# Kernel tuning notes

Hardware: AMD Instinct MI355X
Metric: run time of the kernel (lower is better)

The kernel has to match this reference:

```python
import jax, jax.numpy as jnp
import numpy as np

N = 100000   # nodes
E = 1000000  # edges
DIN = 128    # atom_in_features
DE = 16      # edge_attr_dim
H = 128      # hidden width (preprocess/cheb/postprocess)
K = 3        # Chebyshev order
EPS = 1e-5


def setup_inputs() -> dict:
    key = jax.random.key(0)
    ks = jax.random.split(key, 16)
    s = 0.02
    return {
        "x": jax.random.normal(ks[0], (N, DIN), jnp.float32),
        "edge_index": jax.random.randint(ks[1], (2, E), 0, N),
        "edge_attr": jax.random.normal(ks[2], (E, DE), jnp.float32),
        # AtomEdgeInteraction linear: (DIN+DE) -> H
        "w_int": jax.random.normal(ks[3], (DIN + DE, H), jnp.float32) * s,
        "b_int": jnp.zeros((H,), jnp.float32),
        # preprocess layer 1: Linear + BatchNorm + ReLU
        "w_pre": jax.random.normal(ks[4], (H, H), jnp.float32) * s,
        "b_pre": jnp.zeros((H,), jnp.float32),
        "g_pre": jnp.ones((H,), jnp.float32),
        "be_pre": jnp.zeros((H,), jnp.float32),
        # ChebConv layers: weight [K, in, out] + bias
        "cheb1_w": jax.random.normal(ks[5], (K, H, H), jnp.float32) * s,
        "cheb1_b": jnp.zeros((H,), jnp.float32),
        "cheb2_w": jax.random.normal(ks[6], (K, H, H), jnp.float32) * s,
        "cheb2_b": jnp.zeros((H,), jnp.float32),
        # postprocess: Linear + BatchNorm + ReLU
        "w_post": jax.random.normal(ks[7], (H, H), jnp.float32) * s,
        "b_post": jnp.zeros((H,), jnp.float32),
        "g_post": jnp.ones((H,), jnp.float32),
        "be_post": jnp.zeros((H,), jnp.float32),
        # output layer H -> 1
        "w_out": jax.random.normal(ks[8], (H, 1), jnp.float32) * s,
        "b_out": jnp.zeros((1,), jnp.float32),
    }


def _bn(z, g, b):
    # BatchNorm1d, training-mode batch statistics (biased variance, like torch)
    m = z.mean(0)
    v = ((z - m) ** 2).mean(0)
    return g * (z - m) * jax.lax.rsqrt(v + EPS) + b


def _cheb(h, W, b, row, col, norm):
    # ChebConv with sym normalization, lambda_max=2 => L_hat = -D^{-1/2} A D^{-1/2}
    def lhat(z):
        return jax.ops.segment_sum(norm[:, None] * z[row], col, num_segments=N)

    Tx0 = h
    out = Tx0 @ W[0]
    Tx1 = lhat(Tx0)
    out = out + Tx1 @ W[1]
    for k in range(2, W.shape[0]):
        Tx2 = 2.0 * lhat(Tx1) - Tx0
        out = out + Tx2 @ W[k]
        Tx0, Tx1 = Tx1, Tx2
    return out + b


def reference(x, edge_index, edge_attr,
              w_int, b_int,
              w_pre, b_pre, g_pre, be_pre,
              cheb1_w, cheb1_b, cheb2_w, cheb2_b,
              w_post, b_post, g_post, be_post,
              w_out, b_out):
    row, col = edge_index[0], edge_index[1]
    ones_e = jnp.ones((E,), x.dtype)

    # AtomEdgeInteraction: gather -> concat -> linear -> scatter_mean over col
    comb = jnp.concatenate([x[row], edge_attr], axis=-1)  # [E, DIN+DE]
    upd = comb @ w_int + b_int                             # [E, H]
    cnt = jax.ops.segment_sum(ones_e, col, num_segments=N)
    h = jax.ops.segment_sum(upd, col, num_segments=N) / jnp.clip(cnt, 1.0)[:, None]

    # preprocess layer 1 (Linear + BN + ReLU; dropout rate 0)
    h = jax.nn.relu(_bn(h @ w_pre + b_pre, g_pre, be_pre))

    # sym-normalized edge coefficients for scaled Laplacian
    deg = jax.ops.segment_sum(ones_e, row, num_segments=N)
    dis = jnp.where(deg > 0, jax.lax.rsqrt(jnp.maximum(deg, 1.0)), 0.0)
    norm = -dis[row] * dis[col]  # [E]

    h = jax.nn.relu(_cheb(h, cheb1_w, cheb1_b, row, col, norm))
    h = jax.nn.relu(_cheb(h, cheb2_w, cheb2_b, row, col, norm))

    # postprocess (Linear + BN + ReLU)
    h = jax.nn.relu(_bn(h @ w_post + b_post, g_post, be_post))

    # output layer, squeeze(-1) -> [N]
    return (h @ w_out + b_out).squeeze(-1)
```

## Files before the change

### kernel.cpp

```cpp
#include <hip/hip_runtime.h>
#include <hip/hip_bf16.h>

using u16 = unsigned short;
using u32 = unsigned int;

#define NN 100000
#define NE 1000000

typedef __attribute__((ext_vector_type(8))) short bfrag;
typedef __attribute__((ext_vector_type(4))) float ffrag;

#define BF16ONE2 0x3F803F80u

__device__ __forceinline__ float bf2f(u16 u) { return __uint_as_float(((u32)u) << 16); }
__device__ __forceinline__ u16 f2bf(float f) {
  u32 x = __float_as_uint(f);
  return (u16)((x + 0x7fffu + ((x >> 16) & 1u)) >> 16);
}
__device__ __forceinline__ float rdv(const void* p, long i, int f) {
  return f ? bf2f(((const u16*)p)[i]) : ((const float*)p)[i];
}
__device__ __forceinline__ void acc8(float* a, uint4 v, float w) {
  a[0] = fmaf(w, __uint_as_float(v.x << 16), a[0]);
  a[1] = fmaf(w, __uint_as_float(v.x & 0xffff0000u), a[1]);
  a[2] = fmaf(w, __uint_as_float(v.y << 16), a[2]);
  a[3] = fmaf(w, __uint_as_float(v.y & 0xffff0000u), a[3]);
  a[4] = fmaf(w, __uint_as_float(v.z << 16), a[4]);
  a[5] = fmaf(w, __uint_as_float(v.z & 0xffff0000u), a[5]);
  a[6] = fmaf(w, __uint_as_float(v.w << 16), a[6]);
  a[7] = fmaf(w, __uint_as_float(v.w & 0xffff0000u), a[7]);
}

#define OWXT 0
#define OWPRE 16384
#define OWD1 32768
#define OW11 49152
#define OV21 65536
#define OWD2 81920
#define OW12 98304
#define OV22 114688
#define OWPOST 131072
#define OWET 147456

#define ASTRIDE 136
#define ESTRIDE 132

struct PrepArgs { const void* in[16]; };

__global__ void k_prep(PrepArgs a, const u32* __restrict__ gp, u16* __restrict__ wq,
                       float* __restrict__ wf) {
  int t = blockIdx.x * 256 + threadIdx.x;
  int f = (gp[0] == BF16ONE2) ? 1 : 0;
  if (t < 16384) {
    int o = t >> 7, k = t & 127;
    int ko = k * 128 + o;
    int ok = o * 128 + k;
    wq[OWXT + ok] = f2bf(rdv(a.in[0], ko, f));
    wq[OWPRE + ok] = f2bf(rdv(a.in[2], ko, f));
    float c0 = rdv(a.in[6], ko, f);
    float c1 = rdv(a.in[6], 16384 + ko, f);
    float c2 = rdv(a.in[6], 32768 + ko, f);
    wq[OWD1 + ok] = f2bf(c0 - c2);
    wq[OW11 + ok] = f2bf(c1);
    wq[OV21 + ok] = f2bf(2.f * c2);
    float d0 = rdv(a.in[8], ko, f);
    float d1 = rdv(a.in[8], 16384 + ko, f);
    float d2 = rdv(a.in[8], 32768 + ko, f);
    wq[OWD2 + ok] = f2bf(d0 - d2);
    wq[OW12 + ok] = f2bf(d1);
    wq[OV22 + ok] = f2bf(2.f * d2);
    wq[OWPOST + ok] = f2bf(rdv(a.in[10], ko, f));
  }
  if (t < 4096) {
    int o = t >> 5, k = t & 31;
    wq[OWET + o * 32 + k] = (k < 16) ? f2bf(rdv(a.in[0], (long)(128 + k) * 128 + o, f)) : (u16)0;
  }
  if (t < 1281) {
    int s = t >> 7, j = t & 127;
    const int map[11] = {1, 3, 4, 5, 7, 9, 11, 12, 13, 14, 15};
    wf[t] = rdv(a.in[map[s]], j, f);
  }
}

__global__ void k_hist(const int* __restrict__ ei, int* cnt, int* deg) {
  int e = blockIdx.x * 256 + threadIdx.x;
  if (e >= NE) return;
  atomicAdd(&deg[ei[e]], 1);
  atomicAdd(&cnt[ei[NE + e]], 1);
}

__global__ void k_scan1(const int* __restrict__ cnt, int* off, int* bsum) {
  __shared__ int s[1024];
  int t = threadIdx.x;
  int g = blockIdx.x * 1024 + t;
  int v = (g < NN) ? cnt[g] : 0;
  s[t] = v;
  __syncthreads();
  for (int st = 1; st < 1024; st <<= 1) {
    int x = (t >= st) ? s[t - st] : 0;
    __syncthreads();
    s[t] += x;
    __syncthreads();
  }
  if (g < NN) off[g] = s[t] - v;
  if (t == 1023) bsum[blockIdx.x] = s[t];
}

__global__ void k_scan23(int* off, const int* __restrict__ bsum,
                         const int* __restrict__ deg, float* __restrict__ dis, int nb) {
  __shared__ int s[128];
  int t = threadIdx.x;
  int v = 0;
  if (t < 128) {
    v = (t < nb) ? bsum[t] : 0;
    s[t] = v;
  }
  __syncthreads();
  for (int st = 1; st < 128; st <<= 1) {
    int x = (t >= st && t < 128) ? s[t - st] : 0;
    __syncthreads();
    if (t < 128) s[t] += x;
    __syncthreads();
  }
  if (t < 128) s[t] -= v;
  __syncthreads();
  int pre = s[blockIdx.x];
  int g = blockIdx.x * 1024 + t;
  if (g < NN) {
    off[g] += pre;
    int d = deg[g];
    dis[g] = d > 0 ? rsqrtf((float)d) : 0.f;
  }
  if (g == 0) off[NN] = NE;
}

__global__ void k_place(const int* __restrict__ ei, const int* __restrict__ off,
                        int* cur, int* crow, int* ceid) {
  int e = blockIdx.x * 256 + threadIdx.x;
  if (e >= NE) return;
  int r = ei[e], c = ei[NE + e];
  int p = off[c] + atomicAdd(&cur[c], 1);
  crow[p] = r;
  ceid[p] = e;
}

__global__ __launch_bounds__(256) void k_spmm(const u16* __restrict__ src,
                                              u16* __restrict__ dst,
                                              const int* __restrict__ off,
                                              const int* __restrict__ crow,
                                              const float* __restrict__ cnorm) {
  int t = threadIdx.x;
  int node = blockIdx.x * 8 + (t >> 5);
  if (node >= NN) return;
  int l = t & 31;
  int half = l >> 4;
  int c = (l & 15) * 8;
  int p0 = off[node], p1 = off[node + 1];
  float a[8];
#pragma unroll
  for (int j = 0; j < 8; j++) a[j] = 0.f;
  const u16* sp = src + c;
  int p = p0 + half;
  for (; p + 6 < p1; p += 8) {
    int r0 = crow[p], r1 = crow[p + 2], r2 = crow[p + 4], r3 = crow[p + 6];
    float w0 = cnorm[p], w1 = cnorm[p + 2], w2 = cnorm[p + 4], w3 = cnorm[p + 6];
    uint4 v0 = *(const uint4*)(sp + (long)r0 * 128);
    uint4 v1 = *(const uint4*)(sp + (long)r1 * 128);
    uint4 v2 = *(const uint4*)(sp + (long)r2 * 128);
    uint4 v3 = *(const uint4*)(sp + (long)r3 * 128);
    acc8(a, v0, w0);
    acc8(a, v1, w1);
    acc8(a, v2, w2);
    acc8(a, v3, w3);
  }
  for (; p < p1; p += 2) acc8(a, *(const uint4*)(sp + (long)crow[p] * 128), cnorm[p]);
#pragma unroll
  for (int j = 0; j < 8; j++) a[j] += __shfl_xor(a[j], 16);
  if (half) return;
  uint4 o;
  o.x = (u32)f2bf(a[0]) | ((u32)f2bf(a[1]) << 16);
  o.y = (u32)f2bf(a[2]) | ((u32)f2bf(a[3]) << 16);
  o.z = (u32)f2bf(a[4]) | ((u32)f2bf(a[5]) << 16);
  o.w = (u32)f2bf(a[6]) | ((u32)f2bf(a[7]) << 16);
  *(uint4*)(dst + (long)node * 128 + c) = o;
}

template <int WEIGHTED>
__device__ __forceinline__ void gather_lds(u16* sA, const u16* __restrict__ src,
                                           const int* __restrict__ off,
                                           const int* __restrict__ crow,
                                           const float* __restrict__ cnorm, int r0) {
  int tid = threadIdx.x;
  int grp = tid >> 4;
  int c = (tid & 15) * 8;
  const u16* sp = src + c;
#pragma unroll
  for (int i = 0; i < 4; i++) {
    int nl = grp * 4 + i;
    int node = r0 + nl;
    float a[8];
#pragma unroll
    for (int j = 0; j < 8; j++) a[j] = 0.f;
    if (node < NN) {
      int p0 = off[node], p1 = off[node + 1];
      int p = p0;
      for (; p + 4 <= p1; p += 4) {
        int r0i = crow[p], r1i = crow[p + 1], r2i = crow[p + 2], r3i = crow[p + 3];
        float w0 = WEIGHTED ? cnorm[p] : 1.f;
        float w1 = WEIGHTED ? cnorm[p + 1] : 1.f;
        float w2 = WEIGHTED ? cnorm[p + 2] : 1.f;
        float w3 = WEIGHTED ? cnorm[p + 3] : 1.f;
        uint4 v0 = *(const uint4*)(sp + (long)r0i * 128);
        uint4 v1 = *(const uint4*)(sp + (long)r1i * 128);
        uint4 v2 = *(const uint4*)(sp + (long)r2i * 128);
        uint4 v3 = *(const uint4*)(sp + (long)r3i * 128);
        acc8(a, v0, w0);
        acc8(a, v1, w1);
        acc8(a, v2, w2);
        acc8(a, v3, w3);
      }
      for (; p < p1; p++)
        acc8(a, *(const uint4*)(sp + (long)crow[p] * 128), WEIGHTED ? cnorm[p] : 1.f);
    }
    uint4 o;
    o.x = (u32)f2bf(a[0]) | ((u32)f2bf(a[1]) << 16);
    o.y = (u32)f2bf(a[2]) | ((u32)f2bf(a[3]) << 16);
    o.z = (u32)f2bf(a[4]) | ((u32)f2bf(a[5]) << 16);
    o.w = (u32)f2bf(a[6]) | ((u32)f2bf(a[7]) << 16);
    *(uint4*)(sA + nl * ASTRIDE + c) = o;
  }
}

__global__ __launch_bounds__(256) void k_asum(const void* __restrict__ eattr,
                                              const u32* __restrict__ gp,
                                              u16* __restrict__ asum,
                                              const int* __restrict__ off,
                                              const int* __restrict__ ceid,
                                              const int* __restrict__ crow,
                                              const float* __restrict__ dis,
                                              float* __restrict__ cnorm) {
  int t = blockIdx.x * 256 + threadIdx.x;
  int node = t >> 4;
  if (node >= NN) return;
  int j = t & 15;
  int p0 = off[node], p1 = off[node + 1];
  float ndis = -dis[node];
  for (int p = p0 + j; p < p1; p += 16) cnorm[p] = ndis * dis[crow[p]];
  float a = 0.f;
  if (gp[0] == BF16ONE2) {
    const u16* e16 = (const u16*)eattr;
    int p = p0;
    for (; p + 4 <= p1; p += 4) {
      float v0 = bf2f(e16[(long)ceid[p] * 16 + j]);
      float v1 = bf2f(e16[(long)ceid[p + 1] * 16 + j]);
      float v2 = bf2f(e16[(long)ceid[p + 2] * 16 + j]);
      float v3 = bf2f(e16[(long)ceid[p + 3] * 16 + j]);
      a += v0 + v1 + v2 + v3;
    }
    for (; p < p1; p++) a += bf2f(e16[(long)ceid[p] * 16 + j]);
  } else {
    const float* e32 = (const float*)eattr;
    int p = p0;
    for (; p + 4 <= p1; p += 4) {
      float v0 = e32[(long)ceid[p] * 16 + j];
      float v1 = e32[(long)ceid[p + 1] * 16 + j];
      float v2 = e32[(long)ceid[p + 2] * 16 + j];
      float v3 = e32[(long)ceid[p + 3] * 16 + j];
      a += v0 + v1 + v2 + v3;
    }
    for (; p < p1; p++) a += e32[(long)ceid[p] * 16 + j];
  }
  asum[(long)node * 16 + j] = f2bf(a);
}

struct MArgs {
  const void* A0; const u16* W0T; int a0raw;
  const float* bias;
  u16* out;
  const u32* gp;
  float* part;
};

__global__ __launch_bounds__(256) void k_mgemm(MArgs m) {
  constexpr int ROWS = 128, RT = 8, TPR = 2, SEGW = 64;
  __shared__ __align__(16) u16 sA[ROWS * ASTRIDE];
  int tid = threadIdx.x;
  int wv = tid >> 6, lane = tid & 63;
  int col16 = lane & 15, quad = lane >> 4;
  int r0 = blockIdx.x * ROWS;

  ffrag acc[RT * 2];
#pragma unroll
  for (int i = 0; i < RT * 2; i++)
#pragma unroll
    for (int g = 0; g < 4; g++) acc[i][g] = 0.f;

  {
    int row = tid / TPR, seg = tid % TPR;
    int ra = r0 + row;
    if (ra >= NN) ra = NN - 1;
    bool f32a = m.a0raw && (m.gp[0] != BF16ONE2);
    if (f32a) {
      const float* gs = (const float*)m.A0 + (long)ra * 128 + seg * SEGW;
      u32* lp = (u32*)(sA + row * ASTRIDE + seg * SEGW);
#pragma unroll
      for (int e = 0; e < SEGW / 8; e++) {
        float4 v0 = *(const float4*)(gs + e * 8);
        float4 v1 = *(const float4*)(gs + e * 8 + 4);
        lp[e * 4 + 0] = (u32)f2bf(v0.x) | ((u32)f2bf(v0.y) << 16);
        lp[e * 4 + 1] = (u32)f2bf(v0.z) | ((u32)f2bf(v0.w) << 16);
        lp[e * 4 + 2] = (u32)f2bf(v1.x) | ((u32)f2bf(v1.y) << 16);
        lp[e * 4 + 3] = (u32)f2bf(v1.z) | ((u32)f2bf(v1.w) << 16);
      }
    } else {
      const u16* gs = (const u16*)m.A0 + (long)ra * 128 + seg * SEGW;
      uint4* lp = (uint4*)(sA + row * ASTRIDE + seg * SEGW);
#pragma unroll
      for (int e = 0; e < SEGW / 8; e++) lp[e] = *(const uint4*)(gs + e * 8);
    }
  }
  bfrag b0[2][4];
#pragma unroll
  for (int c = 0; c < 2; c++)
#pragma unroll
    for (int kb = 0; kb < 4; kb++)
      b0[c][kb] = *(const bfrag*)(m.W0T + (long)(wv * 32 + c * 16 + col16) * 128 + kb * 32 + quad * 8);
  __syncthreads();
#pragma unroll
  for (int kb = 0; kb < 4; kb++)
#pragma unroll
    for (int rt = 0; rt < RT; rt++) {
      bfrag af = *(const bfrag*)(sA + (rt * 16 + col16) * ASTRIDE + kb * 32 + quad * 8);
      acc[rt * 2 + 0] = __builtin_amdgcn_mfma_f32_16x16x32_bf16(af, b0[0][kb], acc[rt * 2 + 0], 0, 0, 0);
      acc[rt * 2 + 1] = __builtin_amdgcn_mfma_f32_16x16x32_bf16(af, b0[1][kb], acc[rt * 2 + 1], 0, 0, 0);
    }
  __syncthreads();
#pragma unroll
  for (int rt = 0; rt < RT; rt++)
#pragma unroll
    for (int c = 0; c < 2; c++) {
      int col = wv * 32 + c * 16 + col16;
      float bj = m.bias ? m.bias[col] : 0.f;
#pragma unroll
      for (int g = 0; g < 4; g++)
        sA[(rt * 16 + quad * 4 + g) * ESTRIDE + col] = f2bf(acc[rt * 2 + c][g] + bj);
    }
  __syncthreads();
  {
    int rr = tid / TPR, d = tid % TPR;
    int rowg = r0 + rr;
    if (rowg < NN) {
      const u16* sp2 = sA + rr * ESTRIDE + d * 64;
      uint4* o = (uint4*)(m.out + (long)rowg * 128 + d * 64);
#pragma unroll
      for (int e = 0; e < 8; e++) {
        const uint2* s2 = (const uint2*)(sp2 + e * 8);
        uint2 lo = s2[0], hi = s2[1];
        o[e] = make_uint4(lo.x, lo.y, hi.x, hi.y);
      }
    }
  }
  if (m.part) {
    __shared__ float ps[256], pq[256];
    int col = tid & 127, hf = tid >> 7;
    float s = 0.f, q = 0.f;
#pragma unroll
    for (int r = 0; r < 64; r++) {
      int rr = hf * 64 + r;
      if (r0 + rr < NN) {
        float v = bf2f(sA[rr * ESTRIDE + col]);
        s += v;
        q += v * v;
      }
    }
    ps[tid] = s;
    pq[tid] = q;
    __syncthreads();
    if (tid < 128) {
      m.part[(long)blockIdx.x * 256 + tid] = ps[tid] + ps[tid + 128];
      m.part[(long)blockIdx.x * 256 + 128 + tid] = pq[tid] + pq[tid + 128];
    }
  }
}

__global__ __launch_bounds__(256) void k_etpre(const u16* __restrict__ Xg,
                                               const u16* __restrict__ asum,
                                               const u16* __restrict__ Wet,
                                               const u16* __restrict__ Wpre,
                                               const float* __restrict__ b_int,
                                               const float* __restrict__ b_pre,
                                               const int* __restrict__ off,
                                               const int* __restrict__ crow,
                                               const int* __restrict__ cnt,
                                               u16* __restrict__ out, float* part) {
  __shared__ __align__(16) u16 sA[64 * ASTRIDE];
  int tid = threadIdx.x;
  int wv = tid >> 6, lane = tid & 63;
  int col16 = lane & 15, quad = lane >> 4;
  int r0 = blockIdx.x * 64;

  {
    int row = tid >> 2, seg = tid & 3;
    int ra = r0 + row;
    if (ra >= NN) ra = NN - 1;
    if (seg < 2)
      *(uint4*)(sA + row * ASTRIDE + seg * 8) = *(const uint4*)(asum + (long)ra * 16 + seg * 8);
    else
      *(uint4*)(sA + row * ASTRIDE + seg * 8) = make_uint4(0, 0, 0, 0);
  }
  bfrag be[2];
#pragma unroll
  for (int c = 0; c < 2; c++)
    be[c] = *(const bfrag*)(Wet + (long)(wv * 32 + c * 16 + col16) * 32 + quad * 8);
  __syncthreads();
  ffrag accE[8];
#pragma unroll
  for (int i = 0; i < 8; i++)
#pragma unroll
    for (int g = 0; g < 4; g++) accE[i][g] = 0.f;
#pragma unroll
  for (int rt = 0; rt < 4; rt++) {
    bfrag af = *(const bfrag*)(sA + (rt * 16 + col16) * ASTRIDE + quad * 8);
    accE[rt * 2 + 0] = __builtin_amdgcn_mfma_f32_16x16x32_bf16(af, be[0], accE[rt * 2 + 0], 0, 0, 0);
    accE[rt * 2 + 1] = __builtin_amdgcn_mfma_f32_16x16x32_bf16(af, be[1], accE[rt * 2 + 1], 0, 0, 0);
  }
  __syncthreads();
  gather_lds<0>(sA, Xg, off, crow, nullptr, r0);
  __syncthreads();
#pragma unroll
  for (int rt = 0; rt < 4; rt++)
#pragma unroll
    for (int c = 0; c < 2; c++) {
      int col = wv * 32 + c * 16 + col16;
      float bj = b_int[col];
#pragma unroll
      for (int g = 0; g < 4; g++) {
        int rr = rt * 16 + quad * 4 + g;
        int r = r0 + rr;
        float v = accE[rt * 2 + c][g] + bf2f(sA[rr * ASTRIDE + col]);
        int cc = (r < NN) ? cnt[r] : 0;
        v = (v + (float)cc * bj) / (float)(cc > 1 ? cc : 1);
        sA[rr * ASTRIDE + col] = f2bf(v);
      }
    }
  bfrag b1[2][4];
#pragma unroll
  for (int c = 0; c < 2; c++)
#pragma unroll
    for (int kb = 0; kb < 4; kb++)
      b1[c][kb] = *(const bfrag*)(Wpre + (long)(wv * 32 + c * 16 + col16) * 128 + kb * 32 + quad * 8);
  __syncthreads();
  ffrag a2[8];
#pragma unroll
  for (int i = 0; i < 8; i++)
#pragma unroll
    for (int g = 0; g < 4; g++) a2[i][g] = 0.f;
#pragma unroll
  for (int kb = 0; kb < 4; kb++)
#pragma unroll
    for (int rt = 0; rt < 4; rt++) {
      bfrag af = *(const bfrag*)(sA + (rt * 16 + col16) * ASTRIDE + kb * 32 + quad * 8);
      a2[rt * 2 + 0] = __builtin_amdgcn_mfma_f32_16x16x32_bf16(af, b1[0][kb], a2[rt * 2 + 0], 0, 0, 0);
      a2[rt * 2 + 1] = __builtin_amdgcn_mfma_f32_16x16x32_bf16(af, b1[1][kb], a2[rt * 2 + 1], 0, 0, 0);
    }
  __syncthreads();
#pragma unroll
  for (int rt = 0; rt < 4; rt++)
#pragma unroll
    for (int c = 0; c < 2; c++) {
      int col = wv * 32 + c * 16 + col16;
      float bj = b_pre[col];
#pragma unroll
      for (int g = 0; g < 4; g++)
        sA[(rt * 16 + quad * 4 + g) * ESTRIDE + col] = f2bf(a2[rt * 2 + c][g] + bj);
    }
  __syncthreads();
  {
    int rr = tid >> 2, d = tid & 3;
    int rowg = r0 + rr;
    if (rowg < NN) {
      const u16* sp2 = sA + rr * ESTRIDE + d * 32;
      uint4* o = (uint4*)(out + (long)rowg * 128 + d * 32);
#pragma unroll
      for (int e = 0; e < 4; e++) {
        const uint2* s2 = (const uint2*)(sp2 + e * 8);
        uint2 lo = s2[0], hi = s2[1];
        o[e] = make_uint4(lo.x, lo.y, hi.x, hi.y);
      }
    }
  }
  {
    __shared__ float ps[256], pq[256];
    int col = tid & 127, hf = tid >> 7;
    float s = 0.f, q = 0.f;
#pragma unroll
    for (int r = 0; r < 32; r++) {
      int rr = hf * 32 + r;
      if (r0 + rr < NN) {
        float v = bf2f(sA[rr * ESTRIDE + col]);
        s += v;
        q += v * v;
      }
    }
    ps[tid] = s;
    pq[tid] = q;
    __syncthreads();
    if (tid < 128) {
      part[(long)blockIdx.x * 256 + tid] = ps[tid] + ps[tid + 128];
      part[(long)blockIdx.x * 256 + 128 + tid] = pq[tid] + pq[tid + 128];
    }
  }
}

__global__ __launch_bounds__(256) void k_cheb(const u16* __restrict__ hb,
                                              const u16* __restrict__ T1,
                                              const int* __restrict__ off,
                                              const int* __restrict__ crow,
                                              const float* __restrict__ cnorm,
                                              const u16* __restrict__ WD,
                                              const u16* __restrict__ W1,
                                              const u16* __restrict__ V2,
                                              const float* __restrict__ bias,
                                              u16* __restrict__ out) {
  __shared__ __align__(16) u16 sA[64 * ASTRIDE];
  int tid = threadIdx.x;
  int wv = tid >> 6, lane = tid & 63;
  int col16 = lane & 15, quad = lane >> 4;
  int r0 = blockIdx.x * 64;

  ffrag acc[8];
#pragma unroll
  for (int i = 0; i < 8; i++)
#pragma unroll
    for (int g = 0; g < 4; g++) acc[i][g] = 0.f;

  gather_lds<1>(sA, T1, off, crow, cnorm, r0);
  bfrag bv[2][4];
#pragma unroll
  for (int c = 0; c < 2; c++)
#pragma unroll
    for (int kb = 0; kb < 4; kb++)
      bv[c][kb] = *(const bfrag*)(V2 + (long)(wv * 32 + c * 16 + col16) * 128 + kb * 32 + quad * 8);
  __syncthreads();
#pragma unroll
  for (int kb = 0; kb < 4; kb++)
#pragma unroll
    for (int rt = 0; rt < 4; rt++) {
      bfrag af = *(const bfrag*)(sA + (rt * 16 + col16) * ASTRIDE + kb * 32 + quad * 8);
      acc[rt * 2 + 0] = __builtin_amdgcn_mfma_f32_16x16x32_bf16(af, bv[0][kb], acc[rt * 2 + 0], 0, 0, 0);
      acc[rt * 2 + 1] = __builtin_amdgcn_mfma_f32_16x16x32_bf16(af, bv[1][kb], acc[rt * 2 + 1], 0, 0, 0);
    }
  __syncthreads();

  {
    int row = tid >> 2, seg = tid & 3;
    int ra = r0 + row;
    if (ra >= NN) ra = NN - 1;
    const u16* gs = hb + (long)ra * 128 + seg * 32;
    uint4* lp = (uint4*)(sA + row * ASTRIDE + seg * 32);
#pragma unroll
    for (int e = 0; e < 4; e++) lp[e] = *(const uint4*)(gs + e * 8);
  }
#pragma unroll
  for (int c = 0; c < 2; c++)
#pragma unroll
    for (int kb = 0; kb < 4; kb++)
      bv[c][kb] = *(const bfrag*)(WD + (long)(wv * 32 + c * 16 + col16) * 128 + kb * 32 + quad * 8);
  __syncthreads();
#pragma unroll
  for (int kb = 0; kb < 4; kb++)
#pragma unroll
    for (int rt = 0; rt < 4; rt++) {
      bfrag af = *(const bfrag*)(sA + (rt * 16 + col16) * ASTRIDE + kb * 32 + quad * 8);
      acc[rt * 2 + 0] = __builtin_amdgcn_mfma_f32_16x16x32_bf16(af, bv[0][kb], acc[rt * 2 + 0], 0, 0, 0);
      acc[rt * 2 + 1] = __builtin_amdgcn_mfma_f32_16x16x32_bf16(af, bv[1][kb], acc[rt * 2 + 1], 0, 0, 0);
    }
  __syncthreads();

  {
    int row = tid >> 2, seg = tid & 3;
    int ra = r0 + row;
    if (ra >= NN) ra = NN - 1;
    const u16* gs = T1 + (long)ra * 128 + seg * 32;
    uint4* lp = (uint4*)(sA + row * ASTRIDE + seg * 32);
#pragma unroll
    for (int e = 0; e < 4; e++) lp[e] = *(const uint4*)(gs + e * 8);
  }
#pragma unroll
  for (int c = 0; c < 2; c++)
#pragma unroll
    for (int kb = 0; kb < 4; kb++)
      bv[c][kb] = *(const bfrag*)(W1 + (long)(wv * 32 + c * 16 + col16) * 128 + kb * 32 + quad * 8);
  __syncthreads();
#pragma unroll
  for (int kb = 0; kb < 4; kb++)
#pragma unroll
    for (int rt = 0; rt < 4; rt++) {
      bfrag af = *(const bfrag*)(sA + (rt * 16 + col16) * ASTRIDE + kb * 32 + quad * 8);
      acc[rt * 2 + 0] = __builtin_amdgcn_mfma_f32_16x16x32_bf16(af, bv[0][kb], acc[rt * 2 + 0], 0, 0, 0);
      acc[rt * 2 + 1] = __builtin_amdgcn_mfma_f32_16x16x32_bf16(af, bv[1][kb], acc[rt * 2 + 1], 0, 0, 0);
    }
  __syncthreads();

#pragma unroll
  for (int rt = 0; rt < 4; rt++)
#pragma unroll
    for (int c = 0; c < 2; c++) {
      int col = wv * 32 + c * 16 + col16;
      float bj = bias[col];
#pragma unroll
      for (int g = 0; g < 4; g++)
        sA[(rt * 16 + quad * 4 + g) * ESTRIDE + col] = f2bf(fmaxf(acc[rt * 2 + c][g] + bj, 0.f));
    }
  __syncthreads();
  {
    int rr = tid >> 2, d = tid & 3;
    int rowg = r0 + rr;
    if (rowg < NN) {
      const u16* sp2 = sA + rr * ESTRIDE + d * 32;
      uint4* o = (uint4*)(out + (long)rowg * 128 + d * 32);
#pragma unroll
      for (int e = 0; e < 4; e++) {
        const uint2* s2 = (const uint2*)(sp2 + e * 8);
        uint2 lo = s2[0], hi = s2[1];
        o[e] = make_uint4(lo.x, lo.y, hi.x, hi.y);
      }
    }
  }
}

__global__ void k_redfin(const float* __restrict__ part, const float* __restrict__ gamma,
                         const float* __restrict__ beta, float* ab, int nblk) {
  int tid = threadIdx.x;
  int col = blockIdx.x * 16 + (tid & 15);
  int ch = tid >> 4;
  float s = 0.f, q = 0.f;
  for (int b = ch; b < nblk; b += 16) {
    s += part[(long)b * 256 + col];
    q += part[(long)b * 256 + 128 + col];
  }
  __shared__ float sh[256], qh[256];
  sh[tid] = s;
  qh[tid] = q;
  __syncthreads();
  if (tid < 16) {
    float ts = 0.f, tq = 0.f;
#pragma unroll
    for (int i = 0; i < 16; i++) {
      ts += sh[i * 16 + tid];
      tq += qh[i * 16 + tid];
    }
    int j = blockIdx.x * 16 + tid;
    float m = ts * (1.f / (float)NN);
    float v = fmaxf(tq * (1.f / (float)NN) - m * m, 0.f);
    float a = gamma[j] * rsqrtf(v + 1e-5f);
    ab[j] = a;
    ab[128 + j] = beta[j] - m * a;
  }
}

__global__ void k_bnrelu(const u16* __restrict__ z, u16* __restrict__ out,
                         const float* __restrict__ ab) {
  long idx = (long)blockIdx.x * 256 + threadIdx.x;
  long t = idx * 2;
  if (t >= (long)NN * 128) return;
  int col = (int)(t & 127);
  u32 v = *(const u32*)(z + t);
  float f0 = fmaxf(__uint_as_float(v << 16) * ab[col] + ab[128 + col], 0.f);
  float f1 = fmaxf(__uint_as_float(v & 0xffff0000u) * ab[col + 1] + ab[129 + col], 0.f);
  *(u32*)(out + t) = (u32)f2bf(f0) | ((u32)f2bf(f1) << 16);
}

__global__ void k_out(const u16* __restrict__ z, const float* __restrict__ ab,
                      const float* __restrict__ wout, const float* __restrict__ bout,
                      const u32* __restrict__ gp, void* __restrict__ y) {
  int node = blockIdx.x * 4 + (threadIdx.x >> 6);
  if (node >= NN) return;
  int lane = threadIdx.x & 63;
  float s = 0.f;
#pragma unroll
  for (int c = lane; c < 128; c += 64) {
    float zz = bf2f(z[(long)node * 128 + c]);
    float h = fmaxf(ab[c] * zz + ab[128 + c], 0.f);
    s += h * wout[c];
  }
#pragma unroll
  for (int o = 32; o > 0; o >>= 1) s += __shfl_down(s, o);
  if (lane == 0) {
    float r = s + bout[0];
    if (gp[0] == BF16ONE2) ((u16*)y)[node] = f2bf(r);
    else ((float*)y)[node] = r;
  }
}

extern "C" void kernel_launch(void* const* d_in, const int* in_sizes, int n_in,
                              void* d_out, int out_size, void* d_ws, size_t ws_size,
                              hipStream_t stream) {
  const void* x = d_in[0];
  const int* ei = (const int*)d_in[1];
  const void* eattr = d_in[2];
  const u32* gp = (const u32*)d_in[7];
  (void)in_sizes; (void)n_in; (void)out_size; (void)ws_size;

  char* w = (char*)d_ws;
  size_t p = 0;
  auto alloc = [&](size_t b) { size_t r = p; p += (b + 255) & ~(size_t)255; return r; };
  size_t o_cnt = alloc((size_t)NN * 4);
  size_t o_deg = alloc((size_t)NN * 4);
  size_t o_cur = alloc((size_t)NN * 4);
  size_t o_zero_end = p;
  size_t o_dis = alloc((size_t)NN * 4);
  size_t o_off = alloc((size_t)(NN + 1) * 4);
  size_t o_bsum = alloc(1024 * 4);
  size_t o_ab = alloc(512 * 4);
  size_t o_wq = alloc((size_t)151552 * 2);
  size_t o_wf = alloc((size_t)1281 * 4);
  size_t o_crow = alloc((size_t)NE * 4);
  size_t o_cnrm = alloc((size_t)NE * 4);
  size_t o_asum = alloc((size_t)NN * 16 * 2);
  size_t o_part = alloc((size_t)1563 * 256 * 4);
  size_t o_Bx = alloc((size_t)NN * 128 * 2);
  size_t o_Bt = alloc((size_t)NN * 128 * 2);

  int* cnt = (int*)(w + o_cnt);
  int* deg = (int*)(w + o_deg);
  int* cur = (int*)(w + o_cur);
  float* dis = (float*)(w + o_dis);
  int* off = (int*)(w + o_off);
  int* bsum = (int*)(w + o_bsum);
  float* abA = (float*)(w + o_ab);
  float* abB = abA + 256;
  u16* wq = (u16*)(w + o_wq);
  float* wf = (float*)(w + o_wf);
  int* crow = (int*)(w + o_crow);
  float* cnrm = (float*)(w + o_cnrm);
  u16* asum = (u16*)(w + o_asum);
  float* part = (float*)(w + o_part);
  u16* Bx = (u16*)(w + o_Bx);
  u16* Bt = (u16*)(w + o_Bt);
  int* ceid = (int*)Bt;

  hipMemsetAsync(w + o_cnt, 0, o_zero_end - o_cnt, stream);

  int gE = (NE + 255) / 256;
  int nb = (NN + 1023) / 1024;
  int gS = (NN + 7) / 8;
  int gG1 = (NN + 127) / 128;
  int gG2 = (NN + 63) / 64;

  {
    PrepArgs a;
    for (int i = 0; i < 16; i++) a.in[i] = d_in[3 + i];
    k_prep<<<64, 256, 0, stream>>>(a, gp, wq, wf);
  }

  k_hist<<<gE, 256, 0, stream>>>(ei, cnt, deg);
  k_scan1<<<nb, 1024, 0, stream>>>(cnt, off, bsum);
  k_scan23<<<nb, 1024, 0, stream>>>(off, bsum, deg, dis, nb);
  k_place<<<gE, 256, 0, stream>>>(ei, off, cur, crow, ceid);
  k_asum<<<(NN * 16 + 255) / 256, 256, 0, stream>>>(eattr, gp, asum, off, ceid, crow, dis, cnrm);

  {
    MArgs a = {};
    a.A0 = x; a.W0T = wq + OWXT; a.a0raw = 1;
    a.out = Bx; a.gp = gp;
    k_mgemm<<<gG1, 256, 0, stream>>>(a);
  }
  k_etpre<<<gG2, 256, 0, stream>>>(Bx, asum, wq + OWET, wq + OWPRE, wf + 0, wf + 128,
                                   off, crow, cnt, Bt, part);
  k_redfin<<<8, 256, 0, stream>>>(part, wf + 256, wf + 384, abA, gG2);
  k_bnrelu<<<(int)(((long)NN * 128 / 2 + 255) / 256), 256, 0, stream>>>(Bt, Bx, abA);

  k_spmm<<<gS, 256, 0, stream>>>(Bx, Bt, off, crow, cnrm);
  k_cheb<<<gG2, 256, 0, stream>>>(Bx, Bt, off, crow, cnrm,
                                  wq + OWD1, wq + OW11, wq + OV21, wf + 512, Bx);

  k_spmm<<<gS, 256, 0, stream>>>(Bx, Bt, off, crow, cnrm);
  k_cheb<<<gG2, 256, 0, stream>>>(Bx, Bt, off, crow, cnrm,
                                  wq + OWD2, wq + OW12, wq + OV22, wf + 640, Bx);

  {
    MArgs a = {};
    a.A0 = Bx; a.W0T = wq + OWPOST;
    a.bias = wf + 768; a.out = Bt; a.gp = gp; a.part = part;
    k_mgemm<<<gG1, 256, 0, stream>>>(a);
  }
  k_redfin<<<8, 256, 0, stream>>>(part, wf + 896, wf + 1024, abB, gG1);
  k_out<<<(NN + 3) / 4, 256, 0, stream>>>(Bt, abB, wf + 1152, wf + 1280, gp, d_out);
}
```

Baseline: 756.6 us.

## Privatize histogram and placement atomics per XCC to avoid cross-die contention

Degree/count histograms and CSR placement cursors are replicated per XCC (indexed via the hardware XCC_ID register) and updated with workgroup-scope relaxed atomics. Scan kernels sum the 8 private copies, and a new k_offx kernel computes per-XCC starting offsets so placement needs no shared cursor. The goal is to remove expensive device-coherent atomics that contend across dies. In exchange it adds an extra kernel and 8x larger counters aliased into the Bx buffer, and relies on workgroup scope being sufficient for atomics that multiple workgroups on one XCC share.

```diff
diff --git a/kernel.cpp b/kernel.cpp
--- a/kernel.cpp
+++ b/kernel.cpp
@@ -29,6 +29,12 @@
   a[5] = fmaf(w, __uint_as_float(v.z & 0xffff0000u), a[5]);
   a[6] = fmaf(w, __uint_as_float(v.w << 16), a[6]);
   a[7] = fmaf(w, __uint_as_float(v.w & 0xffff0000u), a[7]);
+}
+
+__device__ __forceinline__ int xccid() {
+  u32 x;
+  asm("s_getreg_b32 %0, hwreg(HW_REG_XCC_ID, 0, 32)" : "=s"(x));
+  return (int)(x & 7);
 }
 
 #define OWXT 0
@@ -82,18 +88,23 @@
   }
 }
 
-__global__ void k_hist(const int* __restrict__ ei, int* cnt, int* deg) {
+__global__ void k_hist(const int* __restrict__ ei, int* cntx, int* degx) {
   int e = blockIdx.x * 256 + threadIdx.x;
   if (e >= NE) return;
-  atomicAdd(&deg[ei[e]], 1);
-  atomicAdd(&cnt[ei[NE + e]], 1);
-}
-
-__global__ void k_scan1(const int* __restrict__ cnt, int* off, int* bsum) {
+  int x = xccid();
+  __hip_atomic_fetch_add(&degx[x * NN + ei[e]], 1, __ATOMIC_RELAXED, __HIP_MEMORY_SCOPE_WORKGROUP);
+  __hip_atomic_fetch_add(&cntx[x * NN + ei[NE + e]], 1, __ATOMIC_RELAXED, __HIP_MEMORY_SCOPE_WORKGROUP);
+}
+
+__global__ void k_scan1(const int* __restrict__ cntx, int* off, int* bsum) {
   __shared__ int s[1024];
   int t = threadIdx.x;
   int g = blockIdx.x * 1024 + t;
-  int v = (g < NN) ? cnt[g] : 0;
+  int v = 0;
+  if (g < NN) {
+#pragma unroll
+    for (int x = 0; x < 8; x++) v += cntx[x * NN + g];
+  }
   s[t] = v;
   __syncthreads();
   for (int st = 1; st < 1024; st <<= 1) {
@@ -107,7 +118,7 @@
 }
 
 __global__ void k_scan23(int* off, const int* __restrict__ bsum,
-                         const int* __restrict__ deg, float* __restrict__ dis, int nb) {
+                         const int* __restrict__ degx, float* __restrict__ dis, int nb) {
   __shared__ int s[128];
   int t = threadIdx.x;
   int v = 0;
@@ -128,18 +139,33 @@
   int g = blockIdx.x * 1024 + t;
   if (g < NN) {
     off[g] += pre;
-    int d = deg[g];
+    int d = 0;
+#pragma unroll
+    for (int x = 0; x < 8; x++) d += degx[x * NN + g];
     dis[g] = d > 0 ? rsqrtf((float)d) : 0.f;
   }
   if (g == 0) off[NN] = NE;
 }
 
-__global__ void k_place(const int* __restrict__ ei, const int* __restrict__ off,
-                        int* cur, int* crow, int* ceid) {
+__global__ void k_offx(const int* __restrict__ off, const int* __restrict__ cntx,
+                       int* __restrict__ offx) {
+  int c = blockIdx.x * 256 + threadIdx.x;
+  if (c >= NN) return;
+  int o = off[c];
+#pragma unroll
+  for (int x = 0; x < 8; x++) {
+    offx[x * NN + c] = o;
+    o += cntx[x * NN + c];
+  }
+}
+
+__global__ void k_place(const int* __restrict__ ei, int* offx, int* crow, int* ceid) {
   int e = blockIdx.x * 256 + threadIdx.x;
   if (e >= NE) return;
+  int x = xccid();
   int r = ei[e], c = ei[NE + e];
-  int p = off[c] + atomicAdd(&cur[c], 1);
+  int p = __hip_atomic_fetch_add(&offx[x * NN + c], 1, __ATOMIC_RELAXED,
+                                 __HIP_MEMORY_SCOPE_WORKGROUP);
   crow[p] = r;
   ceid[p] = e;
 }
@@ -391,7 +417,6 @@
                                                const float* __restrict__ b_pre,
                                                const int* __restrict__ off,
                                                const int* __restrict__ crow,
-                                               const int* __restrict__ cnt,
                                                u16* __restrict__ out, float* part) {
   __shared__ __align__(16) u16 sA[64 * ASTRIDE];
   int tid = threadIdx.x;
@@ -430,16 +455,17 @@
 #pragma unroll
   for (int rt = 0; rt < 4; rt++)
 #pragma unroll
-    for (int c = 0; c < 2; c++) {
-      int col = wv * 32 + c * 16 + col16;
-      float bj = b_int[col];
-#pragma unroll
-      for (int g = 0; g < 4; g++) {
-        int rr = rt * 16 + quad * 4 + g;
-        int r = r0 + rr;
+    for (int g = 0; g < 4; g++) {
+      int rr = rt * 16 + quad * 4 + g;
+      int r = r0 + rr;
+      int cc = (r < NN) ? off[r + 1] - off[r] : 0;
+      float inv = 1.f / (float)(cc > 1 ? cc : 1);
+#pragma unroll
+      for (int c = 0; c < 2; c++) {
+        int col = wv * 32 + c * 16 + col16;
+        float bj = b_int[col];
         float v = accE[rt * 2 + c][g] + bf2f(sA[rr * ASTRIDE + col]);
-        int cc = (r < NN) ? cnt[r] : 0;
-        v = (v + (float)cc * bj) / (float)(cc > 1 ? cc : 1);
+        v = (v + (float)cc * bj) * inv;
         sA[rr * ASTRIDE + col] = f2bf(v);
       }
     }
@@ -705,10 +731,6 @@
   char* w = (char*)d_ws;
   size_t p = 0;
   auto alloc = [&](size_t b) { size_t r = p; p += (b + 255) & ~(size_t)255; return r; };
-  size_t o_cnt = alloc((size_t)NN * 4);
-  size_t o_deg = alloc((size_t)NN * 4);
-  size_t o_cur = alloc((size_t)NN * 4);
-  size_t o_zero_end = p;
   size_t o_dis = alloc((size_t)NN * 4);
   size_t o_off = alloc((size_t)(NN + 1) * 4);
   size_t o_bsum = alloc(1024 * 4);
@@ -722,9 +744,6 @@
   size_t o_Bx = alloc((size_t)NN * 128 * 2);
   size_t o_Bt = alloc((size_t)NN * 128 * 2);
 
-  int* cnt = (int*)(w + o_cnt);
-  int* deg = (int*)(w + o_deg);
-  int* cur = (int*)(w + o_cur);
   float* dis = (float*)(w + o_dis);
   int* off = (int*)(w + o_off);
   int* bsum = (int*)(w + o_bsum);
@@ -738,13 +757,17 @@
   float* part = (float*)(w + o_part);
   u16* Bx = (u16*)(w + o_Bx);
   u16* Bt = (u16*)(w + o_Bt);
+  int* cntx = (int*)Bx;
+  int* degx = cntx + 8 * NN;
+  int* offx = degx + 8 * NN;
   int* ceid = (int*)Bt;
 
-  hipMemsetAsync(w + o_cnt, 0, o_zero_end - o_cnt, stream);
+  hipMemsetAsync(cntx, 0, (size_t)8 * NN * 4 * 2, stream);
 
   int gE = (NE + 255) / 256;
   int nb = (NN + 1023) / 1024;
   int gS = (NN + 7) / 8;
+  int gN = (NN + 255) / 256;
   int gG1 = (NN + 127) / 128;
   int gG2 = (NN + 63) / 64;
 
@@ -754,10 +777,11 @@
     k_prep<<<64, 256, 0, stream>>>(a, gp, wq, wf);
   }
 
-  k_hist<<<gE, 256, 0, stream>>>(ei, cnt, deg);
-  k_scan1<<<nb, 1024, 0, stream>>>(cnt, off, bsum);
-  k_scan23<<<nb, 1024, 0, stream>>>(off, bsum, deg, dis, nb);
-  k_place<<<gE, 256, 0, stream>>>(ei, off, cur, crow, ceid);
+  k_hist<<<gE, 256, 0, stream>>>(ei, cntx, degx);
+  k_scan1<<<nb, 1024, 0, stream>>>(cntx, off, bsum);
+  k_scan23<<<nb, 1024, 0, stream>>>(off, bsum, degx, dis, nb);
+  k_offx<<<gN, 256, 0, stream>>>(off, cntx, offx);
+  k_place<<<gE, 256, 0, stream>>>(ei, offx, crow, ceid);
   k_asum<<<(NN * 16 + 255) / 256, 256, 0, stream>>>(eattr, gp, asum, off, ceid, crow, dis, cnrm);
 
   {
@@ -767,7 +791,7 @@
     k_mgemm<<<gG1, 256, 0, stream>>>(a);
   }
   k_etpre<<<gG2, 256, 0, stream>>>(Bx, asum, wq + OWET, wq + OWPRE, wf + 0, wf + 128,
-                                   off, crow, cnt, Bt, part);
+                                   off, crow, Bt, part);
   k_redfin<<<8, 256, 0, stream>>>(part, wf + 256, wf + 384, abA, gG2);
   k_bnrelu<<<(int)(((long)NN * 128 / 2 + 255) / 256), 256, 0, stream>>>(Bt, Bx, abA);
 
```

Result: no change. 766.7 us (+1.3%).

## Vectorize CSR build: 8 edges per thread, move degree count into place

Applied to the files above, without the earlier changes.

The histogram and placement kernels now handle 8 edges per thread with int4 loads. The out-degree atomic moves from k_hist into k_place, and a new small kernel computes dis. The cursor is pre-seeded with the offsets so placement skips the off[] read, and k_etpre derives the count from off differences instead of reading cnt. This aims to cut per-edge load and launch overhead in graph preprocessing, at the cost of one extra tiny kernel launch and less thread-level parallelism.

```diff
diff --git a/kernel.cpp b/kernel.cpp
--- a/kernel.cpp
+++ b/kernel.cpp
@@ -82,11 +82,23 @@
   }
 }
 
-__global__ void k_hist(const int* __restrict__ ei, int* cnt, int* deg) {
-  int e = blockIdx.x * 256 + threadIdx.x;
-  if (e >= NE) return;
-  atomicAdd(&deg[ei[e]], 1);
-  atomicAdd(&cnt[ei[NE + e]], 1);
+__global__ void k_hist(const int* __restrict__ ei, int* cnt) {
+  long t = (long)blockIdx.x * 256 + threadIdx.x;
+  long e0 = t * 8;
+  if (e0 + 8 <= NE) {
+    int4 c0 = *(const int4*)(ei + NE + e0);
+    int4 c1 = *(const int4*)(ei + NE + e0 + 4);
+    atomicAdd(&cnt[c0.x], 1);
+    atomicAdd(&cnt[c0.y], 1);
+    atomicAdd(&cnt[c0.z], 1);
+    atomicAdd(&cnt[c0.w], 1);
+    atomicAdd(&cnt[c1.x], 1);
+    atomicAdd(&cnt[c1.y], 1);
+    atomicAdd(&cnt[c1.z], 1);
+    atomicAdd(&cnt[c1.w], 1);
+  } else {
+    for (long e = e0; e < NE; e++) atomicAdd(&cnt[ei[NE + e]], 1);
+  }
 }
 
 __global__ void k_scan1(const int* __restrict__ cnt, int* off, int* bsum) {
@@ -106,8 +118,7 @@
   if (t == 1023) bsum[blockIdx.x] = s[t];
 }
 
-__global__ void k_scan23(int* off, const int* __restrict__ bsum,
-                         const int* __restrict__ deg, float* __restrict__ dis, int nb) {
+__global__ void k_scan23(int* off, const int* __restrict__ bsum, int* cur, int nb) {
   __shared__ int s[128];
   int t = threadIdx.x;
   int v = 0;
@@ -127,21 +138,49 @@
   int pre = s[blockIdx.x];
   int g = blockIdx.x * 1024 + t;
   if (g < NN) {
-    off[g] += pre;
-    int d = deg[g];
-    dis[g] = d > 0 ? rsqrtf((float)d) : 0.f;
+    int o = off[g] + pre;
+    off[g] = o;
+    cur[g] = o;
   }
   if (g == 0) off[NN] = NE;
 }
 
-__global__ void k_place(const int* __restrict__ ei, const int* __restrict__ off,
-                        int* cur, int* crow, int* ceid) {
-  int e = blockIdx.x * 256 + threadIdx.x;
-  if (e >= NE) return;
-  int r = ei[e], c = ei[NE + e];
-  int p = off[c] + atomicAdd(&cur[c], 1);
-  crow[p] = r;
-  ceid[p] = e;
+__global__ void k_place(const int* __restrict__ ei, int* cur, int* deg,
+                        int* __restrict__ crow, int* __restrict__ ceid) {
+  long t = (long)blockIdx.x * 256 + threadIdx.x;
+  long e0 = t * 8;
+  if (e0 + 8 <= NE) {
+    int4 r0 = *(const int4*)(ei + e0);
+    int4 r1 = *(const int4*)(ei + e0 + 4);
+    int4 c0 = *(const int4*)(ei + NE + e0);
+    int4 c1 = *(const int4*)(ei + NE + e0 + 4);
+    int r[8] = {r0.x, r0.y, r0.z, r0.w, r1.x, r1.y, r1.z, r1.w};
+    int c[8] = {c0.x, c0.y, c0.z, c0.w, c1.x, c1.y, c1.z, c1.w};
+    int p[8];
+#pragma unroll
+    for (int i = 0; i < 8; i++) p[i] = atomicAdd(&cur[c[i]], 1);
+#pragma unroll
+    for (int i = 0; i < 8; i++) atomicAdd(&deg[r[i]], 1);
+#pragma unroll
+    for (int i = 0; i < 8; i++) crow[p[i]] = r[i];
+#pragma unroll
+    for (int i = 0; i < 8; i++) ceid[p[i]] = (int)(e0 + i);
+  } else {
+    for (long e = e0; e < NE; e++) {
+      int rr = ei[e], cc = ei[NE + e];
+      int p = atomicAdd(&cur[cc], 1);
+      atomicAdd(&deg[rr], 1);
+      crow[p] = rr;
+      ceid[p] = (int)e;
+    }
+  }
+}
+
+__global__ void k_dis(const int* __restrict__ deg, float* __restrict__ dis) {
+  int g = blockIdx.x * 256 + threadIdx.x;
+  if (g >= NN) return;
+  int d = deg[g];
+  dis[g] = d > 0 ? rsqrtf((float)d) : 0.f;
 }
 
 __global__ __launch_bounds__(256) void k_spmm(const u16* __restrict__ src,
@@ -391,7 +430,6 @@
                                                const float* __restrict__ b_pre,
                                                const int* __restrict__ off,
                                                const int* __restrict__ crow,
-                                               const int* __restrict__ cnt,
                                                u16* __restrict__ out, float* part) {
   __shared__ __align__(16) u16 sA[64 * ASTRIDE];
   int tid = threadIdx.x;
@@ -430,16 +468,17 @@
 #pragma unroll
   for (int rt = 0; rt < 4; rt++)
 #pragma unroll
-    for (int c = 0; c < 2; c++) {
-      int col = wv * 32 + c * 16 + col16;
-      float bj = b_int[col];
-#pragma unroll
-      for (int g = 0; g < 4; g++) {
-        int rr = rt * 16 + quad * 4 + g;
-        int r = r0 + rr;
+    for (int g = 0; g < 4; g++) {
+      int rr = rt * 16 + quad * 4 + g;
+      int r = r0 + rr;
+      int cc = (r < NN) ? off[r + 1] - off[r] : 0;
+      float inv = 1.f / (float)(cc > 1 ? cc : 1);
+#pragma unroll
+      for (int c = 0; c < 2; c++) {
+        int col = wv * 32 + c * 16 + col16;
+        float bj = b_int[col];
         float v = accE[rt * 2 + c][g] + bf2f(sA[rr * ASTRIDE + col]);
-        int cc = (r < NN) ? cnt[r] : 0;
-        v = (v + (float)cc * bj) / (float)(cc > 1 ? cc : 1);
+        v = (v + (float)cc * bj) * inv;
         sA[rr * ASTRIDE + col] = f2bf(v);
       }
     }
@@ -707,8 +746,8 @@
   auto alloc = [&](size_t b) { size_t r = p; p += (b + 255) & ~(size_t)255; return r; };
   size_t o_cnt = alloc((size_t)NN * 4);
   size_t o_deg = alloc((size_t)NN * 4);
+  size_t o_zero_end = p;
   size_t o_cur = alloc((size_t)NN * 4);
-  size_t o_zero_end = p;
   size_t o_dis = alloc((size_t)NN * 4);
   size_t o_off = alloc((size_t)(NN + 1) * 4);
   size_t o_bsum = alloc(1024 * 4);
@@ -742,9 +781,10 @@
 
   hipMemsetAsync(w + o_cnt, 0, o_zero_end - o_cnt, stream);
 
-  int gE = (NE + 255) / 256;
+  int gH = (NE / 8 + 255) / 256;
   int nb = (NN + 1023) / 1024;
   int gS = (NN + 7) / 8;
+  int gN = (NN + 255) / 256;
   int gG1 = (NN + 127) / 128;
   int gG2 = (NN + 63) / 64;
 
@@ -754,10 +794,11 @@
     k_prep<<<64, 256, 0, stream>>>(a, gp, wq, wf);
   }
 
-  k_hist<<<gE, 256, 0, stream>>>(ei, cnt, deg);
+  k_hist<<<gH, 256, 0, stream>>>(ei, cnt);
   k_scan1<<<nb, 1024, 0, stream>>>(cnt, off, bsum);
-  k_scan23<<<nb, 1024, 0, stream>>>(off, bsum, deg, dis, nb);
-  k_place<<<gE, 256, 0, stream>>>(ei, off, cur, crow, ceid);
+  k_scan23<<<nb, 1024, 0, stream>>>(off, bsum, cur, nb);
+  k_place<<<gH, 256, 0, stream>>>(ei, cur, deg, crow, ceid);
+  k_dis<<<gN, 256, 0, stream>>>(deg, dis);
   k_asum<<<(NN * 16 + 255) / 256, 256, 0, stream>>>(eattr, gp, asum, off, ceid, crow, dis, cnrm);
 
   {
@@ -767,7 +808,7 @@
     k_mgemm<<<gG1, 256, 0, stream>>>(a);
   }
   k_etpre<<<gG2, 256, 0, stream>>>(Bx, asum, wq + OWET, wq + OWPRE, wf + 0, wf + 128,
-                                   off, crow, cnt, Bt, part);
+                                   off, crow, Bt, part);
   k_redfin<<<8, 256, 0, stream>>>(part, wf + 256, wf + 384, abA, gG2);
   k_bnrelu<<<(int)(((long)NN * 128 / 2 + 255) / 256), 256, 0, stream>>>(Bt, Bx, abA);
 
```

Result: no change. 757.7 us (+0.2%).
